# Kernel tuning notes

Measured on AMD Instinct MI355X. Metric: run time of the kernel, lower is better.

The kernel has to match this reference:

```python
import jax, jax.numpy as jnp
import numpy as np

N_NODES = 10000
K_HOPS = 2
PICKS = 4       # random out-edges per node before symmetrization (~8 avg degree)
D_MAX = 128     # pad width for k-hop neighborhoods
BATCH = 2
F_DIM = 64


def _build_neighborhoods(n, k_hops, picks, d_max, seed=0):
    """Random sparse graph; returns padded k-hop neighborhood indices + lengths.
    Mirrors graphTools.computeNeighborhood: hop-k set = nodes reachable in <=k
    hops, including the node itself."""
    rng = np.random.default_rng(seed)
    nbrs = [set() for _ in range(n)]
    for u in range(n):
        for v in rng.integers(0, n, size=picks):
            v = int(v)
            if v != u:
                nbrs[u].add(v)
                nbrs[v].add(u)
    hop = [{u} | nbrs[u] for u in range(n)]  # 1-hop (incl. self)
    one_hop = hop
    idx = np.empty((k_hops, n, d_max), dtype=np.int32)
    lens = np.empty((k_hops, n), dtype=np.int32)
    for k in range(k_hops):
        if k > 0:
            hop = [set().union(*(one_hop[m] for m in hop[u])) for u in range(n)]
        for u in range(n):
            nb = sorted(hop[u])[:d_max]  # clip (never hit for this graph)
            lens[k, u] = len(nb)
            idx[k, u, :len(nb)] = nb
            idx[k, u, len(nb):] = u  # pad with self (masked out anyway)
    return idx, lens


def setup_inputs() -> dict:
    key = jax.random.key(0)
    kx, kw = jax.random.split(key)
    x = jax.random.normal(kx, (BATCH, F_DIM, N_NODES), dtype=jnp.float32)
    stdv = 1.0 / np.sqrt(K_HOPS)
    weight = jax.random.uniform(kw, (1, K_HOPS + 1), minval=-stdv, maxval=stdv,
                                dtype=jnp.float32)
    idx, lens = _build_neighborhoods(N_NODES, K_HOPS, PICKS, D_MAX)
    return {"x": x, "weight": weight,
            "neigh_idx": jnp.asarray(idx), "neigh_len": jnp.asarray(lens)}


def _masked_median(x, idx, ln):
    # x: [B,F,N]; idx: [N,D]; ln: [N] -> lower median over each ragged set,
    # matching torch.median (element at sorted position (len-1)//2).
    D = idx.shape[1]
    vals = x[:, :, idx]                                   # [B,F,N,D] gather
    mask = jnp.arange(D, dtype=ln.dtype)[None, :] < ln[:, None]  # [N,D]
    vals = jnp.where(mask[None, None], vals, jnp.inf)
    vals = jnp.sort(vals, axis=-1)
    mid = ((ln - 1) // 2).astype(jnp.int32)               # [N]
    med = jnp.take_along_axis(vals, mid[None, None, :, None], axis=-1)
    return med[..., 0]                                    # [B,F,N]


def reference(x, weight, neigh_idx, neigh_len):
    K = neigh_idx.shape[0]
    hops = [x] + [_masked_median(x, neigh_idx[k], neigh_len[k]) for k in range(K)]
    xK = jnp.stack(hops, axis=-1)                         # [B,F,N,K+1]
    return jnp.einsum('bfnk,k->bfn', xK, weight[0])
```

## Files before the change

kernel.cpp:

```cpp
#include <hip/hip_runtime.h>
#include <hip/hip_bf16.h>

constexpr int NN   = 10000;
constexpr int DMAX = 128;
constexpr int ROWS = 128;

__global__ __launch_bounds__(256) void transpose_kernel(
    const float* __restrict__ x, float* __restrict__ xT)
{
    __shared__ float tile[32][33];
    const int n0 = blockIdx.x * 32;
    const int r0 = blockIdx.y * 32;
    const int tx = threadIdx.x;
    const int ty = threadIdx.y;
    #pragma unroll
    for (int i = 0; i < 32; i += 8) {
        const int r = r0 + ty + i;
        const int n = n0 + tx;
        if (n < NN) tile[ty + i][tx] = x[(size_t)r * NN + n];
    }
    __syncthreads();
    #pragma unroll
    for (int i = 0; i < 32; i += 8) {
        const int n = n0 + ty + i;
        const int r = r0 + tx;
        if (n < NN) xT[(size_t)n * ROWS + r] = tile[tx][ty + i];
    }
}

__device__ __forceinline__ float stream_median(const float* __restrict__ xT,
                                               const int* __restrict__ idxp,
                                               int ln, int col)
{
    const float INF  = 1e30f;
    const int   mid  = (ln - 1) >> 1;
    const float midf = (float)mid + 0.5f;
    const float invs = 1.0f / (0.4f * (float)ln);
    float lo = -64.f, hi = 64.f, m = 0.f, x = 0.f;
    float mp = 0.f, cpf = 0.f;
    bool active = true, need_snap = false, have_prev = false;
    int  pass = 0;

    while (__ballot(active) != 0ull) {
        const bool dosnap = (pass >= 1) || (__ballot(need_snap) != 0ull);

        int   c  = 0;
        float mx = -INF, mn = INF;
        if (dosnap) {
            #pragma unroll 4
            for (int j = 0; j < ln; ++j) {
                const float v  = xT[(idxp[j] << 7) + col];
                const bool  le = v <= m;
                c  += le ? 1 : 0;
                mx  = le ? fmaxf(mx, v) : mx;
                mn  = le ? mn : fminf(mn, v);
            }
        } else {
            #pragma unroll 4
            for (int j = 0; j < ln; ++j)
                c += (xT[(idxp[j] << 7) + col] <= m) ? 1 : 0;
        }

        if (active) {
            const float fc = (float)c;
            if (dosnap) {
                need_snap = false;
                if      (c == mid + 1) { x = mx; active = false; }
                else if (c == mid)     { x = mn; active = false; }
                else {
                    if (c > mid + 1) hi = mx; else lo = mn;
                    if (lo >= hi) { x = lo; active = false; }
                    else {
                        const float dd = fc - cpf;
                        float mN = (have_prev && dd != 0.f)
                                 ? m + (midf - fc) * (m - mp) * __builtin_amdgcn_rcpf(dd)
                                 : m + (midf - fc) * invs;
                        mp = m; cpf = fc; have_prev = true;
                        if (!(mN > lo && mN < hi)) mN = 0.5f * (lo + hi);
                        if (mN >= hi) mN = lo;
                        m = mN;
                    }
                }
            } else {
                if (c == mid + 1 || c == mid) {
                    need_snap = true;
                } else {
                    if (c > mid + 1) hi = m; else lo = m;
                    const float dd = fc - cpf;
                    float mN = (have_prev && dd != 0.f)
                             ? m + (midf - fc) * (m - mp) * __builtin_amdgcn_rcpf(dd)
                             : m + (midf - fc) * invs;
                    mp = m; cpf = fc; have_prev = true;
                    if (!(mN > lo && mN < hi)) mN = 0.5f * (lo + hi);
                    if (mN >= hi) mN = lo;
                    m = mN;
                }
            }
        }
        ++pass;
    }
    return x;
}

__global__ __launch_bounds__(128, 8) void median_combine(
    const float* __restrict__ xT, const float* __restrict__ w,
    const int* __restrict__ nidx, const int* __restrict__ nlen,
    float* __restrict__ out)
{
    const int t = threadIdx.x;
    const int n = blockIdx.x;

    float medk[2];
    #pragma unroll
    for (int k = 0; k < 2; ++k) {
        const int ln = nlen[k * NN + n];
        const int* idxp = nidx + ((size_t)k * NN + n) * DMAX;
        medk[k] = stream_median(xT, idxp, ln, t);
    }

    const float xv = xT[(n << 7) + t];
    out[t * NN + n] = w[0] * xv + w[1] * medk[0] + w[2] * medk[1];
}

extern "C" void kernel_launch(void* const* d_in, const int* in_sizes, int n_in,
                              void* d_out, int out_size, void* d_ws, size_t ws_size,
                              hipStream_t stream) {
    const float* x    = (const float*)d_in[0];
    const float* w    = (const float*)d_in[1];
    const int*   nidx = (const int*)d_in[2];
    const int*   nlen = (const int*)d_in[3];
    float* out = (float*)d_out;
    float* xT  = (float*)d_ws;

    dim3 tb(32, 8);
    dim3 tg((NN + 31) / 32, ROWS / 32);
    transpose_kernel<<<tg, tb, 0, stream>>>(x, xT);
    median_combine<<<NN, 128, 0, stream>>>(xT, w, nidx, nlen, out);
}
```

Baseline: 346.3 us.

## Map one wavefront per node with two columns per lane via float2 loads

Each node is now handled by a single 64-lane wavefront, with every lane tracking the median search for two feature columns at once and reading them as one float2. Blocks of 256 threads cover four nodes. The aim is to halve the number of scalar index loads and loop iterations per column and to issue wider memory transactions. The cost is more registers per lane and extra passes, because a lane keeps looping until both of its columns have converged.

```diff
diff --git a/kernel.cpp b/kernel.cpp
--- a/kernel.cpp
+++ b/kernel.cpp
@@ -28,98 +28,111 @@
     }
 }
 
-__device__ __forceinline__ float stream_median(const float* __restrict__ xT,
-                                               const int* __restrict__ idxp,
-                                               int ln, int col)
+__global__ __launch_bounds__(256, 4) void median_combine(
+    const float* __restrict__ xT, const float* __restrict__ w,
+    const int* __restrict__ nidx, const int* __restrict__ nlen,
+    float* __restrict__ out)
 {
-    const float INF  = 1e30f;
-    const int   mid  = (ln - 1) >> 1;
-    const float midf = (float)mid + 0.5f;
-    const float invs = 1.0f / (0.4f * (float)ln);
-    float lo = -64.f, hi = 64.f, m = 0.f, x = 0.f;
-    float mp = 0.f, cpf = 0.f;
-    bool active = true, need_snap = false, have_prev = false;
-    int  pass = 0;
+    const float INF = 1e30f;
+    const int t  = threadIdx.x;
+    const int wv = t >> 6;
+    const int l  = t & 63;
+    const int n  = (blockIdx.x << 2) + wv;
+    const int c0 = l << 1;
 
-    while (__ballot(active) != 0ull) {
-        const bool dosnap = (pass >= 1) || (__ballot(need_snap) != 0ull);
+    float medA[2], medB[2];
 
-        int   c  = 0;
-        float mx = -INF, mn = INF;
-        if (dosnap) {
-            #pragma unroll 4
-            for (int j = 0; j < ln; ++j) {
-                const float v  = xT[(idxp[j] << 7) + col];
-                const bool  le = v <= m;
-                c  += le ? 1 : 0;
-                mx  = le ? fmaxf(mx, v) : mx;
-                mn  = le ? mn : fminf(mn, v);
-            }
-        } else {
-            #pragma unroll 4
-            for (int j = 0; j < ln; ++j)
-                c += (xT[(idxp[j] << 7) + col] <= m) ? 1 : 0;
-        }
+    #pragma unroll
+    for (int k = 0; k < 2; ++k) {
+        const int ln  = nlen[k * NN + n];
+        const int* idxp = nidx + ((size_t)k * NN + n) * DMAX;
+        const int   mid  = (ln - 1) >> 1;
+        const float midf = (float)mid + 0.5f;
+        const float invs = 1.0f / (0.4f * (float)ln);
 
-        if (active) {
-            const float fc = (float)c;
+        float loA = -64.f, hiA = 64.f, mA = 0.f, xA = 0.f, mpA = 0.f, cpA = 0.f;
+        float loB = -64.f, hiB = 64.f, mB = 0.f, xB = 0.f, mpB = 0.f, cpB = 0.f;
+        bool aA = true, aB = true, nsA = false, nsB = false, hpA = false, hpB = false;
+        int pass = 0;
+
+        auto upd = [&](bool dosnap, int cnt, float mx, float mn,
+                       float& lo, float& hi, float& m, float& mp, float& cpf,
+                       float& x, bool& act, bool& ns, bool& hp) {
+            if (!act) return;
+            const float fc = (float)cnt;
             if (dosnap) {
-                need_snap = false;
-                if      (c == mid + 1) { x = mx; active = false; }
-                else if (c == mid)     { x = mn; active = false; }
+                ns = false;
+                if      (cnt == mid + 1) { x = mx; act = false; }
+                else if (cnt == mid)     { x = mn; act = false; }
                 else {
-                    if (c > mid + 1) hi = mx; else lo = mn;
-                    if (lo >= hi) { x = lo; active = false; }
+                    if (cnt > mid + 1) hi = mx; else lo = mn;
+                    if (lo >= hi) { x = lo; act = false; }
                     else {
                         const float dd = fc - cpf;
-                        float mN = (have_prev && dd != 0.f)
+                        float mN = (hp && dd != 0.f)
                                  ? m + (midf - fc) * (m - mp) * __builtin_amdgcn_rcpf(dd)
                                  : m + (midf - fc) * invs;
-                        mp = m; cpf = fc; have_prev = true;
+                        mp = m; cpf = fc; hp = true;
                         if (!(mN > lo && mN < hi)) mN = 0.5f * (lo + hi);
                         if (mN >= hi) mN = lo;
                         m = mN;
                     }
                 }
             } else {
-                if (c == mid + 1 || c == mid) {
-                    need_snap = true;
+                if (cnt == mid + 1 || cnt == mid) {
+                    ns = true;
                 } else {
-                    if (c > mid + 1) hi = m; else lo = m;
+                    if (cnt > mid + 1) hi = m; else lo = m;
                     const float dd = fc - cpf;
-                    float mN = (have_prev && dd != 0.f)
+                    float mN = (hp && dd != 0.f)
                              ? m + (midf - fc) * (m - mp) * __builtin_amdgcn_rcpf(dd)
                              : m + (midf - fc) * invs;
-                    mp = m; cpf = fc; have_prev = true;
+                    mp = m; cpf = fc; hp = true;
                     if (!(mN > lo && mN < hi)) mN = 0.5f * (lo + hi);
                     if (mN >= hi) mN = lo;
                     m = mN;
                 }
             }
+        };
+
+        while (__ballot(aA || aB) != 0ull) {
+            const bool dosnap = (pass >= 1) || (__ballot(nsA || nsB) != 0ull);
+
+            int   cntA = 0, cntB = 0;
+            float mxA = -INF, mnA = INF, mxB = -INF, mnB = INF;
+            if (dosnap) {
+                #pragma unroll 4
+                for (int j = 0; j < ln; ++j) {
+                    const float2 v = *reinterpret_cast<const float2*>(
+                        xT + (idxp[j] << 7) + c0);
+                    const bool leA = v.x <= mA, leB = v.y <= mB;
+                    cntA += leA ? 1 : 0;
+                    mxA = leA ? fmaxf(mxA, v.x) : mxA;  mnA = leA ? mnA : fminf(mnA, v.x);
+                    cntB += leB ? 1 : 0;
+                    mxB = leB ? fmaxf(mxB, v.y) : mxB;  mnB = leB ? mnB : fminf(mnB, v.y);
+                }
+            } else {
+                #pragma unroll 4
+                for (int j = 0; j < ln; ++j) {
+                    const float2 v = *reinterpret_cast<const float2*>(
+                        xT + (idxp[j] << 7) + c0);
+                    cntA += (v.x <= mA) ? 1 : 0;
+                    cntB += (v.y <= mB) ? 1 : 0;
+                }
+            }
+
+            upd(dosnap, cntA, mxA, mnA, loA, hiA, mA, mpA, cpA, xA, aA, nsA, hpA);
+            upd(dosnap, cntB, mxB, mnB, loB, hiB, mB, mpB, cpB, xB, aB, nsB, hpB);
+            ++pass;
         }
-        ++pass;
-    }
-    return x;
-}
-
-__global__ __launch_bounds__(128, 8) void median_combine(
-    const float* __restrict__ xT, const float* __restrict__ w,
-    const int* __restrict__ nidx, const int* __restrict__ nlen,
-    float* __restrict__ out)
-{
-    const int t = threadIdx.x;
-    const int n = blockIdx.x;
-
-    float medk[2];
-    #pragma unroll
-    for (int k = 0; k < 2; ++k) {
-        const int ln = nlen[k * NN + n];
-        const int* idxp = nidx + ((size_t)k * NN + n) * DMAX;
-        medk[k] = stream_median(xT, idxp, ln, t);
+        medA[k] = xA;
+        medB[k] = xB;
     }
 
-    const float xv = xT[(n << 7) + t];
-    out[t * NN + n] = w[0] * xv + w[1] * medk[0] + w[2] * medk[1];
+    const float2 xv = *reinterpret_cast<const float2*>(xT + (n << 7) + c0);
+    const float w0 = w[0], w1 = w[1], w2 = w[2];
+    out[(size_t)c0 * NN + n]       = w0 * xv.x + w1 * medA[0] + w2 * medA[1];
+    out[(size_t)(c0 + 1) * NN + n] = w0 * xv.y + w1 * medB[0] + w2 * medB[1];
 }
 
 extern "C" void kernel_launch(void* const* d_in, const int* in_sizes, int n_in,
@@ -135,5 +148,5 @@
     dim3 tb(32, 8);
     dim3 tg((NN + 31) / 32, ROWS / 32);
     transpose_kernel<<<tg, tb, 0, stream>>>(x, xT);
-    median_combine<<<NN, 128, 0, stream>>>(xT, w, nidx, nlen, out);
+    median_combine<<<NN / 4, 256, 0, stream>>>(xT, w, nidx, nlen, out);
 }
```

Result: slower. 422.2 us (+21.9%).
